# Kernel tuning notes

Hardware: AMD Instinct MI355X
Metric: run time of the kernel (lower is better)

Reference implementation:

```python
import jax, jax.numpy as jnp
import numpy as np

B, H, W = 2, 64, 1024
C1, C2 = 64, 128
MLP = [128, 128]
KH, KW = 5, 5
NS = 3
DIST = 100.0
BN_EPS = 1e-5


def setup_inputs() -> dict:
    key = jax.random.key(0)
    ks = jax.random.split(key, 12)
    inp = {
        "xyz1_proj": jax.random.normal(ks[0], (B, H, W, 3), jnp.float32),
        "xyz2_proj": jax.random.normal(ks[1], (B, H, W, 3), jnp.float32),
        "feat1_proj": jax.random.normal(ks[2], (B, H, W, C1), jnp.float32),
        "feat2_proj": jax.random.normal(ks[3], (B, H, W, C2), jnp.float32),
    }
    cin = C1 + C2
    chans = [cin] + MLP
    for i in range(len(MLP)):
        inp[f"w{i}"] = jax.random.normal(ks[4 + 2 * i], (chans[i], chans[i + 1]), jnp.float32) * 0.05
        inp[f"b{i}"] = jnp.zeros((chans[i + 1],), jnp.float32)
        inp[f"g{i}"] = jnp.ones((chans[i + 1],), jnp.float32)
        inp[f"be{i}"] = jnp.zeros((chans[i + 1],), jnp.float32)
    return inp


def _grid_knn(xyz1, xyz2):
    """Structured-grid KNN (no_sort_knn): for each query pixel, scan a KHxKW
    window in row-major order and take the first NS in-bounds neighbors whose
    squared distance is below DIST^2. Returns flat neighbor indices (B,N,NS)
    and a validity mask (B,N,NS,1)."""
    b, h, w, _ = xyz1.shape
    n = h * w
    k = KH * KW
    x1 = xyz1.reshape(b, n, 3)
    x2 = xyz2.reshape(b, n, 3)
    oh = jnp.repeat(jnp.arange(KH) - KH // 2, KW)   # (K,)
    ow = jnp.tile(jnp.arange(KW) - KW // 2, KH)     # (K,)
    nh = jnp.arange(h)[:, None, None] + oh[None, None, :]   # (H,1,K)
    nw = jnp.arange(w)[None, :, None] + ow[None, None, :]   # (1,W,K)
    inb = ((nh >= 0) & (nh < h)) & ((nw >= 0) & (nw < w))    # (H,W,K)
    flat = jnp.clip(nh, 0, h - 1) * w + jnp.clip(nw, 0, w - 1)
    flat = jnp.broadcast_to(flat, (h, w, k)).reshape(n, k)
    inb = jnp.broadcast_to(inb, (h, w, k)).reshape(n, k)
    # window gather: (B,N,K,3)
    neigh = jnp.take(x2, flat.reshape(-1), axis=1).reshape(b, n, k, 3)
    sq = jnp.sum(jnp.square(neigh - x1[:, :, None, :]), -1)  # (B,N,K)
    valid = inb[None] & (sq < DIST * DIST)
    v = valid.astype(jnp.int32)
    rank = jnp.cumsum(v, -1) - v  # rank among valid, scan order
    sel, fnd = [], []
    for j in range(NS):
        hit = valid & (rank == j)
        sel.append(jnp.argmax(hit, -1))
        fnd.append(jnp.any(hit, -1))
    sel = jnp.stack(sel, -1)          # (B,N,NS) window slot
    found = jnp.stack(fnd, -1)        # (B,N,NS)
    flat_b = jnp.broadcast_to(flat[None], (b, n, k))
    sel_flat = jnp.take_along_axis(flat_b, sel, axis=-1)
    sel_flat = jnp.where(found, sel_flat, 0)  # zeros like the init buffers
    mask = found.astype(x1.dtype)[..., None]  # (B,N,NS,1)
    return sel_flat, mask


def _gather(feat_flat, sel_flat):
    # feat_flat: (B,N,C), sel_flat: (B,N,NS) -> (B,N,NS,C)
    b, n, c = feat_flat.shape
    idx = sel_flat.reshape(b, n * NS, 1)
    g = jnp.take_along_axis(feat_flat, jnp.broadcast_to(idx, (b, n * NS, c)), axis=1)
    return g.reshape(b, n, NS, c)


def reference(xyz1_proj, xyz2_proj, feat1_proj, feat2_proj,
              w0, b0, g0, be0, w1, b1, g1, be1):
    b, h, w, _ = xyz1_proj.shape
    n = h * w
    xyz1 = xyz1_proj.reshape(b, n, 3)
    xyz2 = xyz2_proj.reshape(b, n, 3)
    feat2 = feat2_proj.reshape(b, n, -1)

    sel_flat, mask = _grid_knn(xyz1_proj, xyz2_proj)
    mask = jax.lax.stop_gradient(mask)

    grouped_xyz = _gather(xyz2, sel_flat) * mask          # (B,N,NS,3)
    grouped_feat = _gather(feat2, sel_flat) * mask        # (B,N,NS,C2)

    dist = jnp.sum(jnp.square(grouped_xyz - xyz1[:, :, None, :]), -1)  # (B,N,NS)
    dist = jnp.where(dist < 1e-10, jnp.full_like(dist, 1e-10), dist)
    norm = jnp.sum(1.0 / dist, axis=2, keepdims=True)     # (B,N,1)
    weight = (1.0 / dist) / norm                          # (B,N,NS)
    interp = jnp.sum(grouped_feat * weight[..., None], axis=2)  # (B,N,C2)

    x = jnp.concatenate([feat1_proj.reshape(b, n, -1), interp], -1)  # (B,N,C1+C2)

    # 1x1 conv MLP with training-mode BatchNorm + ReLU
    for (wi, bi, gi, bei) in ((w0, b0, g0, be0), (w1, b1, g1, be1)):
        x = x @ wi + bi
        mu = jnp.mean(x, axis=(0, 1))
        var = jnp.var(x, axis=(0, 1))
        x = (x - mu) * jax.lax.rsqrt(var + BN_EPS) * gi + bei
        x = jax.nn.relu(x)
    return x  # (B, H*W, MLP[-1])
```

## Files before the change

kernel.cpp:

```cpp
#include <hip/hip_runtime.h>

#define H_    64
#define W_    1024
#define NPT   65536
#define NTOT  131072
#define C1_   64
#define C2_   128
#define CIN_  192
#define CM_   128
#define NS_   3
#define DIST2_ 10000.0f
#define BN_EPS_ 1e-5f
#define NSLOT 32

typedef __attribute__((ext_vector_type(8))) short short8;
typedef __attribute__((ext_vector_type(4))) float floatx4;

static __device__ __forceinline__ unsigned short f2bf(float f) {
    unsigned int u = __float_as_uint(f);
    u += 0x7fffu + ((u >> 16) & 1u);
    return (unsigned short)(u >> 16);
}
static __device__ __forceinline__ float bflo(unsigned u) { return __uint_as_float(u << 16); }
static __device__ __forceinline__ float bfhi(unsigned u) { return __uint_as_float(u & 0xffff0000u); }
static __device__ __forceinline__ unsigned packbf(float a, float b) {
    return (unsigned)f2bf(a) | ((unsigned)f2bf(b) << 16);
}

__global__ __launch_bounds__(256) void prep_knn_kernel(
    const float* __restrict__ w0, const float* __restrict__ w1,
    const float* __restrict__ xyz1, const float* __restrict__ xyz2,
    unsigned short* __restrict__ w0F, unsigned short* __restrict__ w1F,
    int* __restrict__ sel, float* __restrict__ wgt)
{
    const int blk = blockIdx.x;
    if (blk < 20) {
        int tid = blk * 256 + threadIdx.x;
        if (tid < 3072) {
            int c = tid, lane = c & 63, nt = (c >> 6) & 7, kk = c >> 9;
            int n = nt * 16 + (lane & 15);
            int kb = kk * 32 + (lane >> 4) * 8;
            #pragma unroll
            for (int j = 0; j < 8; j++)
                w0F[(size_t)c * 8 + j] = f2bf(w0[(size_t)(kb + j) * CM_ + n]);
        } else if (tid < 5120) {
            int c = tid - 3072, lane = c & 63, nt = (c >> 6) & 7, kk = c >> 9;
            int n = nt * 16 + (lane & 15);
            int kb = kk * 32 + (lane >> 4) * 8;
            #pragma unroll
            for (int j = 0; j < 8; j++)
                w1F[(size_t)c * 8 + j] = f2bf(w1[(size_t)(kb + j) * CM_ + n]);
        }
        return;
    }

    int pt = (blk - 20) * 256 + threadIdx.x;
    if (pt >= NTOT) return;
    int bidx = pt / NPT, n = pt % NPT;
    int h = n / W_, w = n % W_;

    const float* p1 = xyz1 + (size_t)pt * 3;
    float x1 = p1[0], y1 = p1[1], z1 = p1[2];
    const float* x2b = xyz2 + (size_t)bidx * NPT * 3;

    int   s0 = 0, s1 = 0, s2 = 0;
    float d0 = 0.f, d1 = 0.f, d2 = 0.f;
    int cnt = 0;
    for (int dh = -2; dh <= 2; dh++) {
        int nh = h + dh;
        bool okh = (nh >= 0) && (nh < H_);
        for (int dw = -2; dw <= 2; dw++) {
            int nw = w + dw;
            if (!(okh && nw >= 0 && nw < W_)) continue;
            int nidx = nh * W_ + nw;
            const float* p2 = x2b + (size_t)nidx * 3;
            float dx = p2[0] - x1, dy = p2[1] - y1, dz = p2[2] - z1;
            float sq = dx * dx + dy * dy + dz * dz;
            if (sq < DIST2_ && cnt < NS_) {
                if (cnt == 0)      { s0 = nidx; d0 = sq; }
                else if (cnt == 1) { s1 = nidx; d1 = sq; }
                else               { s2 = nidx; d2 = sq; }
                cnt++;
            }
        }
    }
    float self2 = x1 * x1 + y1 * y1 + z1 * z1;
    float dd0 = (cnt > 0) ? d0 : self2;
    float dd1 = (cnt > 1) ? d1 : self2;
    float dd2 = (cnt > 2) ? d2 : self2;
    dd0 = fmaxf(dd0, 1e-10f); dd1 = fmaxf(dd1, 1e-10f); dd2 = fmaxf(dd2, 1e-10f);
    float i0 = 1.0f / dd0, i1 = 1.0f / dd1, i2 = 1.0f / dd2;
    float norm = i0 + i1 + i2;
    sel[(size_t)pt * NS_ + 0] = (cnt > 0) ? s0 : 0;
    sel[(size_t)pt * NS_ + 1] = (cnt > 1) ? s1 : 0;
    sel[(size_t)pt * NS_ + 2] = (cnt > 2) ? s2 : 0;
    wgt[(size_t)pt * NS_ + 0] = (cnt > 0) ? i0 / norm : 0.f;
    wgt[(size_t)pt * NS_ + 1] = (cnt > 1) ? i1 / norm : 0.f;
    wgt[(size_t)pt * NS_ + 2] = (cnt > 2) ? i2 / norm : 0.f;
}

__global__ __launch_bounds__(128) void bnfin_kernel(
    const float* __restrict__ slots, const float* __restrict__ g,
    const float* __restrict__ be, float* __restrict__ bnp)
{
    int t = threadIdx.x;
    float s = 0.f, q2 = 0.f;
    #pragma unroll
    for (int sl = 0; sl < NSLOT; sl++) {
        s  += slots[sl * 256 + t];
        q2 += slots[sl * 256 + CM_ + t];
    }
    const float invn = 1.0f / (float)NTOT;
    float mu = s * invn, var = q2 * invn - mu * mu;
    float sc = g[t] * rsqrtf(var + BN_EPS_);
    bnp[t] = sc;
    bnp[CM_ + t] = be[t] - mu * sc;
}

__global__ __launch_bounds__(256, 3) void fused1_kernel(
    const float* __restrict__ feat1, const float* __restrict__ feat2,
    const int* __restrict__ sel, const float* __restrict__ wgt,
    const unsigned short* __restrict__ w0F, const float* __restrict__ b0,
    uint2* __restrict__ y0w, float* __restrict__ slots0)
{
    __shared__ unsigned short xstage[128][CM_ + 8];
    __shared__ int   selL[128][NS_];
    __shared__ float wgtL[128][NS_];
    __shared__ float wsum[4][CM_], wsq[4][CM_];

    const int t = threadIdx.x;
    const int blk = blockIdx.x;
    const int pbase = blk * 128;
    const int bidx = blk >> 9;
    const int wv = t >> 6, lane = t & 63;
    const int m = lane & 15, q = lane >> 4;
    const int row0 = pbase + wv * 16 + m;
    const int row1 = row0 + 64;

    #pragma unroll
    for (int i = 0; i < 2; i++) {
        int idx = t + i * 256;
        if (idx < 128 * NS_) {
            ((int*)selL)[idx]   = sel[(size_t)pbase * NS_ + idx];
            ((float*)wgtL)[idx] = wgt[(size_t)pbase * NS_ + idx];
        }
    }

    short8 af0[2], af1[2];
    #pragma unroll
    for (int kk = 0; kk < 2; kk++) {
        const float* s0p = feat1 + (size_t)row0 * C1_ + kk * 32 + q * 8;
        const float* s1p = feat1 + (size_t)row1 * C1_ + kk * 32 + q * 8;
        float4 fa = *(const float4*)(s0p), fb = *(const float4*)(s0p + 4);
        float4 ga = *(const float4*)(s1p), gb = *(const float4*)(s1p + 4);
        short8 a, b;
        a[0] = f2bf(fa.x); a[1] = f2bf(fa.y); a[2] = f2bf(fa.z); a[3] = f2bf(fa.w);
        a[4] = f2bf(fb.x); a[5] = f2bf(fb.y); a[6] = f2bf(fb.z); a[7] = f2bf(fb.w);
        b[0] = f2bf(ga.x); b[1] = f2bf(ga.y); b[2] = f2bf(ga.z); b[3] = f2bf(ga.w);
        b[4] = f2bf(gb.x); b[5] = f2bf(gb.y); b[6] = f2bf(gb.z); b[7] = f2bf(gb.w);
        af0[kk] = a; af1[kk] = b;
    }
    __syncthreads();

    const float* f2b = feat2 + (size_t)bidx * NPT * C2_;
    #pragma unroll
    for (int i = 0; i < 16; i++) {
        int idx = t + i * 256;
        int p = idx >> 5, c4 = (idx & 31) << 2;
        float ax = 0.f, ay = 0.f, az = 0.f, aw = 0.f;
        #pragma unroll
        for (int j = 0; j < NS_; j++) {
            float wj = wgtL[p][j];
            const float4 f = *(const float4*)(f2b + (size_t)selL[p][j] * C2_ + c4);
            ax += wj * f.x; ay += wj * f.y; az += wj * f.z; aw += wj * f.w;
        }
        ushort4 u;
        u.x = f2bf(ax); u.y = f2bf(ay); u.z = f2bf(az); u.w = f2bf(aw);
        *(ushort4*)&xstage[p][c4] = u;
    }
    __syncthreads();

    floatx4 acc0[8], acc1[8];
    #pragma unroll
    for (int nt = 0; nt < 8; nt++) {
        acc0[nt] = (floatx4){0.f, 0.f, 0.f, 0.f};
        acc1[nt] = (floatx4){0.f, 0.f, 0.f, 0.f};
    }

    const int lr0 = wv * 16 + m, lr1 = lr0 + 64;
    #pragma unroll
    for (int kk = 0; kk < 6; kk++) {
        short8 bw[8];
        #pragma unroll
        for (int nt = 0; nt < 8; nt++)
            bw[nt] = *(const short8*)(w0F + ((size_t)(kk * 8 + nt) * 64 + lane) * 8);
        short8 a0, a1;
        if (kk < 2) { a0 = af0[kk]; a1 = af1[kk]; }
        else {
            a0 = *(const short8*)&xstage[lr0][(kk - 2) * 32 + q * 8];
            a1 = *(const short8*)&xstage[lr1][(kk - 2) * 32 + q * 8];
        }
        #pragma unroll
        for (int nt = 0; nt < 8; nt++) {
            acc0[nt] = __builtin_amdgcn_mfma_f32_16x16x32_bf16(a0, bw[nt], acc0[nt], 0, 0, 0);
            acc1[nt] = __builtin_amdgcn_mfma_f32_16x16x32_bf16(a1, bw[nt], acc1[nt], 0, 0, 0);
        }
    }

    #pragma unroll
    for (int nt = 0; nt < 8; nt++) {
        int n = nt * 16 + m;
        float bv = b0[n];
        unsigned u0 = packbf(acc0[nt][0] + bv, acc0[nt][1] + bv);
        unsigned u1 = packbf(acc0[nt][2] + bv, acc0[nt][3] + bv);
        unsigned u2 = packbf(acc1[nt][0] + bv, acc1[nt][1] + bv);
        unsigned u3 = packbf(acc1[nt][2] + bv, acc1[nt][3] + bv);
        int g0i = blk * 2;
        y0w[((size_t)(g0i * 4 + wv) * 8 + nt) * 64 + lane]       = make_uint2(u0, u1);
        y0w[((size_t)((g0i + 1) * 4 + wv) * 8 + nt) * 64 + lane] = make_uint2(u2, u3);
        float v0 = bflo(u0), v1 = bfhi(u0), v2 = bflo(u1), v3 = bfhi(u1);
        float v4 = bflo(u2), v5 = bfhi(u2), v6 = bflo(u3), v7 = bfhi(u3);
        float s  = v0 + v1 + v2 + v3 + v4 + v5 + v6 + v7;
        float q2 = v0*v0 + v1*v1 + v2*v2 + v3*v3 + v4*v4 + v5*v5 + v6*v6 + v7*v7;
        s += __shfl_xor(s, 16, 64); q2 += __shfl_xor(q2, 16, 64);
        s += __shfl_xor(s, 32, 64); q2 += __shfl_xor(q2, 32, 64);
        if (q == 0) { wsum[wv][n] = s; wsq[wv][n] = q2; }
    }
    __syncthreads();

    float* slot = slots0 + (size_t)(blk & (NSLOT - 1)) * 256;
    if (t < CM_)
        atomicAdd(&slot[t], wsum[0][t] + wsum[1][t] + wsum[2][t] + wsum[3][t]);
    else
        atomicAdd(&slot[t], wsq[0][t - CM_] + wsq[1][t - CM_] + wsq[2][t - CM_] + wsq[3][t - CM_]);
}

__global__ __launch_bounds__(256, 3) void fused2_kernel(
    const uint2* __restrict__ y0w, const float* __restrict__ bnp0,
    const unsigned short* __restrict__ w1F, const float* __restrict__ b1,
    uint2* __restrict__ y1w, float* __restrict__ slots1)
{
    __shared__ unsigned short x1s[128][CM_ + 8];
    __shared__ float wsum[4][CM_], wsq[4][CM_];

    const int t = threadIdx.x;
    const int blk = blockIdx.x;
    const int wv = t >> 6, lane = t & 63;
    const int m = lane & 15, q = lane >> 4;
    const int g0i = blk * 2;

    #pragma unroll
    for (int nt = 0; nt < 8; nt++) {
        int n = nt * 16 + m;
        float sc = bnp0[n], sh = bnp0[CM_ + n];
        uint2 ua = y0w[((size_t)(g0i * 4 + wv) * 8 + nt) * 64 + lane];
        uint2 ub = y0w[((size_t)((g0i + 1) * 4 + wv) * 8 + nt) * 64 + lane];
        int rb = wv * 16 + q * 4;
        x1s[rb + 0][n] = f2bf(fmaxf(bflo(ua.x) * sc + sh, 0.f));
        x1s[rb + 1][n] = f2bf(fmaxf(bfhi(ua.x) * sc + sh, 0.f));
        x1s[rb + 2][n] = f2bf(fmaxf(bflo(ua.y) * sc + sh, 0.f));
        x1s[rb + 3][n] = f2bf(fmaxf(bfhi(ua.y) * sc + sh, 0.f));
        x1s[64 + rb + 0][n] = f2bf(fmaxf(bflo(ub.x) * sc + sh, 0.f));
        x1s[64 + rb + 1][n] = f2bf(fmaxf(bfhi(ub.x) * sc + sh, 0.f));
        x1s[64 + rb + 2][n] = f2bf(fmaxf(bflo(ub.y) * sc + sh, 0.f));
        x1s[64 + rb + 3][n] = f2bf(fmaxf(bfhi(ub.y) * sc + sh, 0.f));
    }
    __syncthreads();

    const int lr0 = wv * 16 + m, lr1 = lr0 + 64;
    floatx4 acc0[8], acc1[8];
    #pragma unroll
    for (int nt = 0; nt < 8; nt++) {
        acc0[nt] = (floatx4){0.f, 0.f, 0.f, 0.f};
        acc1[nt] = (floatx4){0.f, 0.f, 0.f, 0.f};
    }

    #pragma unroll
    for (int kk = 0; kk < 4; kk++) {
        short8 bw[8];
        #pragma unroll
        for (int nt = 0; nt < 8; nt++)
            bw[nt] = *(const short8*)(w1F + ((size_t)(kk * 8 + nt) * 64 + lane) * 8);
        short8 a0 = *(const short8*)&x1s[lr0][kk * 32 + q * 8];
        short8 a1 = *(const short8*)&x1s[lr1][kk * 32 + q * 8];
        #pragma unroll
        for (int nt = 0; nt < 8; nt++) {
            acc0[nt] = __builtin_amdgcn_mfma_f32_16x16x32_bf16(a0, bw[nt], acc0[nt], 0, 0, 0);
            acc1[nt] = __builtin_amdgcn_mfma_f32_16x16x32_bf16(a1, bw[nt], acc1[nt], 0, 0, 0);
        }
    }

    #pragma unroll
    for (int nt = 0; nt < 8; nt++) {
        int n = nt * 16 + m;
        float bv = b1[n];
        unsigned u0 = packbf(acc0[nt][0] + bv, acc0[nt][1] + bv);
        unsigned u1 = packbf(acc0[nt][2] + bv, acc0[nt][3] + bv);
        unsigned u2 = packbf(acc1[nt][0] + bv, acc1[nt][1] + bv);
        unsigned u3 = packbf(acc1[nt][2] + bv, acc1[nt][3] + bv);
        y1w[((size_t)(g0i * 4 + wv) * 8 + nt) * 64 + lane]       = make_uint2(u0, u1);
        y1w[((size_t)((g0i + 1) * 4 + wv) * 8 + nt) * 64 + lane] = make_uint2(u2, u3);
        float v0 = bflo(u0), v1 = bfhi(u0), v2 = bflo(u1), v3 = bfhi(u1);
        float v4 = bflo(u2), v5 = bfhi(u2), v6 = bflo(u3), v7 = bfhi(u3);
        float s  = v0 + v1 + v2 + v3 + v4 + v5 + v6 + v7;
        float q2 = v0*v0 + v1*v1 + v2*v2 + v3*v3 + v4*v4 + v5*v5 + v6*v6 + v7*v7;
        s += __shfl_xor(s, 16, 64); q2 += __shfl_xor(q2, 16, 64);
        s += __shfl_xor(s, 32, 64); q2 += __shfl_xor(q2, 32, 64);
        if (q == 0) { wsum[wv][n] = s; wsq[wv][n] = q2; }
    }
    __syncthreads();

    float* slot = slots1 + (size_t)(blk & (NSLOT - 1)) * 256;
    if (t < CM_)
        atomicAdd(&slot[t], wsum[0][t] + wsum[1][t] + wsum[2][t] + wsum[3][t]);
    else
        atomicAdd(&slot[t], wsq[0][t - CM_] + wsq[1][t - CM_] + wsq[2][t - CM_] + wsq[3][t - CM_]);
}

__global__ __launch_bounds__(256) void bn_out_kernel(
    const uint2* __restrict__ y1w, const float* __restrict__ bnp1,
    float* __restrict__ out)
{
    __shared__ float xo[64][CM_ + 12];
    const int t = threadIdx.x;
    const int blk = blockIdx.x;
    const int wv = t >> 6, lane = t & 63;
    const int m = lane & 15, q = lane >> 4;

    #pragma unroll
    for (int nt = 0; nt < 8; nt++) {
        int n = nt * 16 + m;
        float sc = bnp1[n], sh = bnp1[CM_ + n];
        uint2 u = y1w[((size_t)(blk * 4 + wv) * 8 + nt) * 64 + lane];
        int rb = wv * 16 + q * 4;
        xo[rb + 0][n] = fmaxf(bflo(u.x) * sc + sh, 0.f);
        xo[rb + 1][n] = fmaxf(bfhi(u.x) * sc + sh, 0.f);
        xo[rb + 2][n] = fmaxf(bflo(u.y) * sc + sh, 0.f);
        xo[rb + 3][n] = fmaxf(bfhi(u.y) * sc + sh, 0.f);
    }
    __syncthreads();

    const int pbase = blk * 64;
    #pragma unroll
    for (int i = 0; i < 8; i++) {
        int idx = t + i * 256;
        int p = idx >> 5, c4 = (idx & 31) << 2;
        float4 v = *(const float4*)&xo[p][c4];
        *(float4*)(out + (size_t)(pbase + p) * CM_ + c4) = v;
    }
}

extern "C" void kernel_launch(void* const* d_in, const int* in_sizes, int n_in,
                              void* d_out, int out_size, void* d_ws, size_t ws_size,
                              hipStream_t stream)
{
    const float* xyz1  = (const float*)d_in[0];
    const float* xyz2  = (const float*)d_in[1];
    const float* feat1 = (const float*)d_in[2];
    const float* feat2 = (const float*)d_in[3];
    const float* w0    = (const float*)d_in[4];
    const float* b0    = (const float*)d_in[5];
    const float* g0    = (const float*)d_in[6];
    const float* be0   = (const float*)d_in[7];
    const float* w1    = (const float*)d_in[8];
    const float* b1    = (const float*)d_in[9];
    const float* g1    = (const float*)d_in[10];
    const float* be1   = (const float*)d_in[11];
    float* out = (float*)d_out;

    char* ws = (char*)d_ws;
    float* slots0       = (float*)(ws);
    float* slots1       = (float*)(ws + (size_t)NSLOT * 256 * 4);
    float* bnp0         = (float*)(ws + 2 * (size_t)NSLOT * 256 * 4);
    float* bnp1         = bnp0 + 256;
    char*  p            = (char*)(bnp1 + 256);
    int*   sel          = (int*)p;             p += (size_t)NTOT * NS_ * 4;
    float* wgt          = (float*)p;           p += (size_t)NTOT * NS_ * 4;
    unsigned short* w0F = (unsigned short*)p;  p += (size_t)CIN_ * CM_ * 2;
    unsigned short* w1F = (unsigned short*)p;  p += (size_t)CM_ * CM_ * 2;
    uint2* y0w          = (uint2*)p;           p += (size_t)NTOT * CM_ * 2;
    uint2* y1w          = (uint2*)p;

    hipMemsetAsync(ws, 0, 2 * (size_t)NSLOT * 256 * 4, stream);

    prep_knn_kernel<<<20 + NTOT / 256, 256, 0, stream>>>(w0, w1, xyz1, xyz2,
                                                         w0F, w1F, sel, wgt);
    fused1_kernel<<<NTOT / 128, 256, 0, stream>>>(feat1, feat2, sel, wgt,
                                                  w0F, b0, y0w, slots0);
    bnfin_kernel<<<1, 128, 0, stream>>>(slots0, g0, be0, bnp0);
    fused2_kernel<<<NTOT / 128, 256, 0, stream>>>(y0w, bnp0, w1F, b1, y1w, slots1);
    bnfin_kernel<<<1, 128, 0, stream>>>(slots1, g1, be1, bnp1);
    bn_out_kernel<<<NTOT / 64, 256, 0, stream>>>(y1w, bnp1, out);
}
```

Baseline: 221.6 us.

## Fuse KNN into first GEMM kernel and BN finalize into consumers

Moves the grid KNN search and inverse-distance weight computation into fused1_kernel, so each block computes neighbor indices and weights directly into shared memory instead of going through global sel/wgt buffers. The two single-block BN-finalize kernels are removed; every block of fused2 and bn_out now reduces the 32 stat slots itself. bn_out processes two 64-row tiles per block. This cuts kernel launches and global round-trips, but adds serial KNN latency on half the threads of each fused1 block and redundant slot reductions in every block.

```diff
diff --git a/kernel.cpp b/kernel.cpp
--- a/kernel.cpp
+++ b/kernel.cpp
@@ -27,99 +27,31 @@
     return (unsigned)f2bf(a) | ((unsigned)f2bf(b) << 16);
 }
 
-__global__ __launch_bounds__(256) void prep_knn_kernel(
+__global__ __launch_bounds__(256) void prepw_kernel(
     const float* __restrict__ w0, const float* __restrict__ w1,
+    unsigned short* __restrict__ w0F, unsigned short* __restrict__ w1F)
+{
+    int tid = blockIdx.x * 256 + threadIdx.x;
+    if (tid < 3072) {
+        int c = tid, lane = c & 63, nt = (c >> 6) & 7, kk = c >> 9;
+        int n = nt * 16 + (lane & 15);
+        int kb = kk * 32 + (lane >> 4) * 8;
+        #pragma unroll
+        for (int j = 0; j < 8; j++)
+            w0F[(size_t)c * 8 + j] = f2bf(w0[(size_t)(kb + j) * CM_ + n]);
+    } else if (tid < 5120) {
+        int c = tid - 3072, lane = c & 63, nt = (c >> 6) & 7, kk = c >> 9;
+        int n = nt * 16 + (lane & 15);
+        int kb = kk * 32 + (lane >> 4) * 8;
+        #pragma unroll
+        for (int j = 0; j < 8; j++)
+            w1F[(size_t)c * 8 + j] = f2bf(w1[(size_t)(kb + j) * CM_ + n]);
+    }
+}
+
+__global__ __launch_bounds__(256, 3) void fused1_kernel(
     const float* __restrict__ xyz1, const float* __restrict__ xyz2,
-    unsigned short* __restrict__ w0F, unsigned short* __restrict__ w1F,
-    int* __restrict__ sel, float* __restrict__ wgt)
-{
-    const int blk = blockIdx.x;
-    if (blk < 20) {
-        int tid = blk * 256 + threadIdx.x;
-        if (tid < 3072) {
-            int c = tid, lane = c & 63, nt = (c >> 6) & 7, kk = c >> 9;
-            int n = nt * 16 + (lane & 15);
-            int kb = kk * 32 + (lane >> 4) * 8;
-            #pragma unroll
-            for (int j = 0; j < 8; j++)
-                w0F[(size_t)c * 8 + j] = f2bf(w0[(size_t)(kb + j) * CM_ + n]);
-        } else if (tid < 5120) {
-            int c = tid - 3072, lane = c & 63, nt = (c >> 6) & 7, kk = c >> 9;
-            int n = nt * 16 + (lane & 15);
-            int kb = kk * 32 + (lane >> 4) * 8;
-            #pragma unroll
-            for (int j = 0; j < 8; j++)
-                w1F[(size_t)c * 8 + j] = f2bf(w1[(size_t)(kb + j) * CM_ + n]);
-        }
-        return;
-    }
-
-    int pt = (blk - 20) * 256 + threadIdx.x;
-    if (pt >= NTOT) return;
-    int bidx = pt / NPT, n = pt % NPT;
-    int h = n / W_, w = n % W_;
-
-    const float* p1 = xyz1 + (size_t)pt * 3;
-    float x1 = p1[0], y1 = p1[1], z1 = p1[2];
-    const float* x2b = xyz2 + (size_t)bidx * NPT * 3;
-
-    int   s0 = 0, s1 = 0, s2 = 0;
-    float d0 = 0.f, d1 = 0.f, d2 = 0.f;
-    int cnt = 0;
-    for (int dh = -2; dh <= 2; dh++) {
-        int nh = h + dh;
-        bool okh = (nh >= 0) && (nh < H_);
-        for (int dw = -2; dw <= 2; dw++) {
-            int nw = w + dw;
-            if (!(okh && nw >= 0 && nw < W_)) continue;
-            int nidx = nh * W_ + nw;
-            const float* p2 = x2b + (size_t)nidx * 3;
-            float dx = p2[0] - x1, dy = p2[1] - y1, dz = p2[2] - z1;
-            float sq = dx * dx + dy * dy + dz * dz;
-            if (sq < DIST2_ && cnt < NS_) {
-                if (cnt == 0)      { s0 = nidx; d0 = sq; }
-                else if (cnt == 1) { s1 = nidx; d1 = sq; }
-                else               { s2 = nidx; d2 = sq; }
-                cnt++;
-            }
-        }
-    }
-    float self2 = x1 * x1 + y1 * y1 + z1 * z1;
-    float dd0 = (cnt > 0) ? d0 : self2;
-    float dd1 = (cnt > 1) ? d1 : self2;
-    float dd2 = (cnt > 2) ? d2 : self2;
-    dd0 = fmaxf(dd0, 1e-10f); dd1 = fmaxf(dd1, 1e-10f); dd2 = fmaxf(dd2, 1e-10f);
-    float i0 = 1.0f / dd0, i1 = 1.0f / dd1, i2 = 1.0f / dd2;
-    float norm = i0 + i1 + i2;
-    sel[(size_t)pt * NS_ + 0] = (cnt > 0) ? s0 : 0;
-    sel[(size_t)pt * NS_ + 1] = (cnt > 1) ? s1 : 0;
-    sel[(size_t)pt * NS_ + 2] = (cnt > 2) ? s2 : 0;
-    wgt[(size_t)pt * NS_ + 0] = (cnt > 0) ? i0 / norm : 0.f;
-    wgt[(size_t)pt * NS_ + 1] = (cnt > 1) ? i1 / norm : 0.f;
-    wgt[(size_t)pt * NS_ + 2] = (cnt > 2) ? i2 / norm : 0.f;
-}
-
-__global__ __launch_bounds__(128) void bnfin_kernel(
-    const float* __restrict__ slots, const float* __restrict__ g,
-    const float* __restrict__ be, float* __restrict__ bnp)
-{
-    int t = threadIdx.x;
-    float s = 0.f, q2 = 0.f;
-    #pragma unroll
-    for (int sl = 0; sl < NSLOT; sl++) {
-        s  += slots[sl * 256 + t];
-        q2 += slots[sl * 256 + CM_ + t];
-    }
-    const float invn = 1.0f / (float)NTOT;
-    float mu = s * invn, var = q2 * invn - mu * mu;
-    float sc = g[t] * rsqrtf(var + BN_EPS_);
-    bnp[t] = sc;
-    bnp[CM_ + t] = be[t] - mu * sc;
-}
-
-__global__ __launch_bounds__(256, 3) void fused1_kernel(
     const float* __restrict__ feat1, const float* __restrict__ feat2,
-    const int* __restrict__ sel, const float* __restrict__ wgt,
     const unsigned short* __restrict__ w0F, const float* __restrict__ b0,
     uint2* __restrict__ y0w, float* __restrict__ slots0)
 {
@@ -137,13 +69,47 @@
     const int row0 = pbase + wv * 16 + m;
     const int row1 = row0 + 64;
 
-    #pragma unroll
-    for (int i = 0; i < 2; i++) {
-        int idx = t + i * 256;
-        if (idx < 128 * NS_) {
-            ((int*)selL)[idx]   = sel[(size_t)pbase * NS_ + idx];
-            ((float*)wgtL)[idx] = wgt[(size_t)pbase * NS_ + idx];
-        }
+    if (t < 128) {
+        int pt = pbase + t;
+        int n = pt & (NPT - 1);
+        int h = n >> 10, w = n & (W_ - 1);
+        const float* p1 = xyz1 + (size_t)pt * 3;
+        float x1 = p1[0], y1 = p1[1], z1 = p1[2];
+        const float* x2b = xyz2 + (size_t)bidx * NPT * 3;
+        int s0 = 0, s1 = 0, s2 = 0;
+        float d0 = 0.f, d1 = 0.f, d2 = 0.f;
+        int cnt = 0;
+        for (int dh = -2; dh <= 2; dh++) {
+            int nh = h + dh;
+            bool okh = (nh >= 0) && (nh < H_);
+            for (int dw = -2; dw <= 2; dw++) {
+                int nw = w + dw;
+                if (!(okh && nw >= 0 && nw < W_)) continue;
+                int nidx = nh * W_ + nw;
+                const float* p2 = x2b + (size_t)nidx * 3;
+                float dx = p2[0] - x1, dy = p2[1] - y1, dz = p2[2] - z1;
+                float sq = dx * dx + dy * dy + dz * dz;
+                if (sq < DIST2_ && cnt < NS_) {
+                    if (cnt == 0)      { s0 = nidx; d0 = sq; }
+                    else if (cnt == 1) { s1 = nidx; d1 = sq; }
+                    else               { s2 = nidx; d2 = sq; }
+                    cnt++;
+                }
+            }
+        }
+        float self2 = x1 * x1 + y1 * y1 + z1 * z1;
+        float dd0 = (cnt > 0) ? d0 : self2;
+        float dd1 = (cnt > 1) ? d1 : self2;
+        float dd2 = (cnt > 2) ? d2 : self2;
+        dd0 = fmaxf(dd0, 1e-10f); dd1 = fmaxf(dd1, 1e-10f); dd2 = fmaxf(dd2, 1e-10f);
+        float i0 = 1.0f / dd0, i1 = 1.0f / dd1, i2 = 1.0f / dd2;
+        float norm = i0 + i1 + i2;
+        selL[t][0] = (cnt > 0) ? s0 : 0;
+        selL[t][1] = (cnt > 1) ? s1 : 0;
+        selL[t][2] = (cnt > 2) ? s2 : 0;
+        wgtL[t][0] = (cnt > 0) ? i0 / norm : 0.f;
+        wgtL[t][1] = (cnt > 1) ? i1 / norm : 0.f;
+        wgtL[t][2] = (cnt > 2) ? i2 / norm : 0.f;
     }
 
     short8 af0[2], af1[2];
@@ -236,11 +202,13 @@
 }
 
 __global__ __launch_bounds__(256, 3) void fused2_kernel(
-    const uint2* __restrict__ y0w, const float* __restrict__ bnp0,
+    const uint2* __restrict__ y0w, const float* __restrict__ slots0,
+    const float* __restrict__ g0, const float* __restrict__ be0,
     const unsigned short* __restrict__ w1F, const float* __restrict__ b1,
     uint2* __restrict__ y1w, float* __restrict__ slots1)
 {
     __shared__ unsigned short x1s[128][CM_ + 8];
+    __shared__ float scl[CM_], shf[CM_];
     __shared__ float wsum[4][CM_], wsq[4][CM_];
 
     const int t = threadIdx.x;
@@ -249,10 +217,24 @@
     const int m = lane & 15, q = lane >> 4;
     const int g0i = blk * 2;
 
+    if (t < CM_) {
+        float s = 0.f, q2 = 0.f;
+        #pragma unroll
+        for (int sl = 0; sl < NSLOT; sl++) {
+            s  += slots0[sl * 256 + t];
+            q2 += slots0[sl * 256 + CM_ + t];
+        }
+        const float invn = 1.0f / (float)NTOT;
+        float mu = s * invn, var = q2 * invn - mu * mu;
+        float sc = g0[t] * rsqrtf(var + BN_EPS_);
+        scl[t] = sc; shf[t] = be0[t] - mu * sc;
+    }
+    __syncthreads();
+
     #pragma unroll
     for (int nt = 0; nt < 8; nt++) {
         int n = nt * 16 + m;
-        float sc = bnp0[n], sh = bnp0[CM_ + n];
+        float sc = scl[n], sh = shf[n];
         uint2 ua = y0w[((size_t)(g0i * 4 + wv) * 8 + nt) * 64 + lane];
         uint2 ub = y0w[((size_t)((g0i + 1) * 4 + wv) * 8 + nt) * 64 + lane];
         int rb = wv * 16 + q * 4;
@@ -318,35 +300,55 @@
 }
 
 __global__ __launch_bounds__(256) void bn_out_kernel(
-    const uint2* __restrict__ y1w, const float* __restrict__ bnp1,
+    const uint2* __restrict__ y1w, const float* __restrict__ slots1,
+    const float* __restrict__ g1, const float* __restrict__ be1,
     float* __restrict__ out)
 {
     __shared__ float xo[64][CM_ + 12];
+    __shared__ float scl[CM_], shf[CM_];
     const int t = threadIdx.x;
     const int blk = blockIdx.x;
     const int wv = t >> 6, lane = t & 63;
     const int m = lane & 15, q = lane >> 4;
 
-    #pragma unroll
-    for (int nt = 0; nt < 8; nt++) {
-        int n = nt * 16 + m;
-        float sc = bnp1[n], sh = bnp1[CM_ + n];
-        uint2 u = y1w[((size_t)(blk * 4 + wv) * 8 + nt) * 64 + lane];
-        int rb = wv * 16 + q * 4;
-        xo[rb + 0][n] = fmaxf(bflo(u.x) * sc + sh, 0.f);
-        xo[rb + 1][n] = fmaxf(bfhi(u.x) * sc + sh, 0.f);
-        xo[rb + 2][n] = fmaxf(bflo(u.y) * sc + sh, 0.f);
-        xo[rb + 3][n] = fmaxf(bfhi(u.y) * sc + sh, 0.f);
-    }
-    __syncthreads();
-
-    const int pbase = blk * 64;
-    #pragma unroll
-    for (int i = 0; i < 8; i++) {
-        int idx = t + i * 256;
-        int p = idx >> 5, c4 = (idx & 31) << 2;
-        float4 v = *(const float4*)&xo[p][c4];
-        *(float4*)(out + (size_t)(pbase + p) * CM_ + c4) = v;
+    if (t < CM_) {
+        float s = 0.f, q2 = 0.f;
+        #pragma unroll
+        for (int sl = 0; sl < NSLOT; sl++) {
+            s  += slots1[sl * 256 + t];
+            q2 += slots1[sl * 256 + CM_ + t];
+        }
+        const float invn = 1.0f / (float)NTOT;
+        float mu = s * invn, var = q2 * invn - mu * mu;
+        float sc = g1[t] * rsqrtf(var + BN_EPS_);
+        scl[t] = sc; shf[t] = be1[t] - mu * sc;
+    }
+    __syncthreads();
+
+    #pragma unroll
+    for (int tile = 0; tile < 2; tile++) {
+        const int g = blk * 2 + tile;
+        #pragma unroll
+        for (int nt = 0; nt < 8; nt++) {
+            int n = nt * 16 + m;
+            float sc = scl[n], sh = shf[n];
+            uint2 u = y1w[((size_t)(g * 4 + wv) * 8 + nt) * 64 + lane];
+            int rb = wv * 16 + q * 4;
+            xo[rb + 0][n] = fmaxf(bflo(u.x) * sc + sh, 0.f);
+            xo[rb + 1][n] = fmaxf(bfhi(u.x) * sc + sh, 0.f);
+            xo[rb + 2][n] = fmaxf(bflo(u.y) * sc + sh, 0.f);
+            xo[rb + 3][n] = fmaxf(bfhi(u.y) * sc + sh, 0.f);
+        }
+        __syncthreads();
+        const int pbase = g * 64;
+        #pragma unroll
+        for (int i = 0; i < 8; i++) {
+            int idx = t + i * 256;
+            int p = idx >> 5, c4 = (idx & 31) << 2;
+            float4 v = *(const float4*)&xo[p][c4];
+            *(float4*)(out + (size_t)(pbase + p) * CM_ + c4) = v;
+        }
+        __syncthreads();
     }
 }
 
@@ -371,11 +373,7 @@
     char* ws = (char*)d_ws;
     float* slots0       = (float*)(ws);
     float* slots1       = (float*)(ws + (size_t)NSLOT * 256 * 4);
-    float* bnp0         = (float*)(ws + 2 * (size_t)NSLOT * 256 * 4);
-    float* bnp1         = bnp0 + 256;
-    char*  p            = (char*)(bnp1 + 256);
-    int*   sel          = (int*)p;             p += (size_t)NTOT * NS_ * 4;
-    float* wgt          = (float*)p;           p += (size_t)NTOT * NS_ * 4;
+    char*  p            = ws + 2 * (size_t)NSLOT * 256 * 4;
     unsigned short* w0F = (unsigned short*)p;  p += (size_t)CIN_ * CM_ * 2;
     unsigned short* w1F = (unsigned short*)p;  p += (size_t)CM_ * CM_ * 2;
     uint2* y0w          = (uint2*)p;           p += (size_t)NTOT * CM_ * 2;
@@ -383,12 +381,10 @@
 
     hipMemsetAsync(ws, 0, 2 * (size_t)NSLOT * 256 * 4, stream);
 
-    prep_knn_kernel<<<20 + NTOT / 256, 256, 0, stream>>>(w0, w1, xyz1, xyz2,
-                                                         w0F, w1F, sel, wgt);
-    fused1_kernel<<<NTOT / 128, 256, 0, stream>>>(feat1, feat2, sel, wgt,
+    prepw_kernel<<<20, 256, 0, stream>>>(w0, w1, w0F, w1F);
+    fused1_kernel<<<NTOT / 128, 256, 0, stream>>>(xyz1, xyz2, feat1, feat2,
                                                   w0F, b0, y0w, slots0);
-    bnfin_kernel<<<1, 128, 0, stream>>>(slots0, g0, be0, bnp0);
-    fused2_kernel<<<NTOT / 128, 256, 0, stream>>>(y0w, bnp0, w1F, b1, y1w, slots1);
-    bnfin_kernel<<<1, 128, 0, stream>>>(slots1, g1, be1, bnp1);
-    bn_out_kernel<<<NTOT / 64, 256, 0, stream>>>(y1w, bnp1, out);
-}
+    fused2_kernel<<<NTOT / 128, 256, 0, stream>>>(y0w, slots0, g0, be0,
+                                                  w1F, b1, y1w, slots1);
+    bn_out_kernel<<<NTOT / 128, 256, 0, stream>>>(y1w, slots1, g1, be1, out);
+}
```

Measured after the change: 227.0 us. 2.4% more time.
